# Optimization experiments

Hardware: AMD Instinct MI355X
Metric: run time of the kernel (lower is better)

The kernel has to match this reference:

```python
import jax, jax.numpy as jnp
import numpy as np

ALPHA = 0.01  # 1 / tau, tau=100, dt=None

def setup_inputs() -> dict:
    key = jax.random.key(0)
    ks = jax.random.split(key, 3)
    T, B, I, H = 256, 64, 512, 2048
    x = jax.random.normal(ks[0], (T, B, I), dtype=jnp.float32)
    # PyTorch Linear init scale ~ 1/sqrt(fan_in)
    W_ih = jax.random.normal(ks[1], (H, I), dtype=jnp.float32) / np.sqrt(I)
    b_ih = jnp.zeros((H,), dtype=jnp.float32)
    W_hh = jax.random.normal(ks[2], (H, H), dtype=jnp.float32) / np.sqrt(H)
    b_hh = jnp.zeros((H,), dtype=jnp.float32)
    return {"x": x, "W_ih": W_ih, "b_ih": b_ih, "W_hh": W_hh, "b_hh": b_hh}

def reference(x, W_ih, b_ih, W_hh, b_hh):
    # x: [T, B, I]; leaky CTRNN recurrence, time-major scan.
    T, B, I = x.shape
    H = W_hh.shape[0]
    # Precompute input projection for all timesteps in one GEMM: [T, B, H]
    xin = jnp.einsum('tbi,hi->tbh', x, W_ih) + b_ih
    h0 = jnp.zeros((B, H), dtype=x.dtype)

    def step(h, xt):
        h_new = jax.nn.relu(xt + h @ W_hh.T + b_hh)
        h = (1.0 - ALPHA) * h + ALPHA * h_new
        return h, h

    h_last, out = jax.lax.scan(step, h0, xin)
    return out, h_last
```

## Files before the change

kernel.cpp:

```cpp
#include <hip/hip_runtime.h>

#define T_DIM 256
#define B_DIM 64
#define I_DIM 512
#define H_DIM 2048
#define BH (B_DIM * H_DIM)
#define NBLK 256
#define PUB_U64 32768

typedef __attribute__((ext_vector_type(8))) short bf16x8;
typedef __attribute__((ext_vector_type(4))) float f32x4;

__device__ __forceinline__ unsigned aloadU32(const unsigned* p) {
  return __hip_atomic_load(p, __ATOMIC_RELAXED, __HIP_MEMORY_SCOPE_AGENT);
}
__device__ __forceinline__ unsigned long long aload64(
    const unsigned long long* p) {
  return __hip_atomic_load(p, __ATOMIC_RELAXED, __HIP_MEMORY_SCOPE_AGENT);
}
__device__ __forceinline__ void astore4(float* p, float a) {
  union { unsigned u; float f; } c; c.f = a;
  __hip_atomic_store((unsigned*)p, c.u, __ATOMIC_RELAXED,
                     __HIP_MEMORY_SCOPE_AGENT);
}
__device__ __forceinline__ void astoreU(unsigned long long* p,
                                        unsigned long long v) {
  __hip_atomic_store(p, v, __ATOMIC_RELAXED, __HIP_MEMORY_SCOPE_AGENT);
}

__device__ __forceinline__ unsigned bf16_rne(float x) {
  union { float f; unsigned u; } c; c.f = x;
  return (c.u + 0x7FFFu + ((c.u >> 16) & 1u)) >> 16;
}
__device__ __forceinline__ float bf16_to_f(unsigned b) {
  union { float f; unsigned u; } c; c.u = b << 16; return c.f;
}
__device__ __forceinline__ void cvt_pair(float x0, float x1,
                                         unsigned& hi, unsigned& lo) {
  unsigned h0 = bf16_rne(x0), h1 = bf16_rne(x1);
  float r0 = x0 - bf16_to_f(h0), r1 = x1 - bf16_to_f(h1);
  unsigned l0 = bf16_rne(r0), l1 = bf16_rne(r1);
  hi = h0 | (h1 << 16);
  lo = l0 | (l1 << 16);
}
__device__ __forceinline__ void cvt8(const float* s, uint4& hi, uint4& lo) {
  float4 a = *(const float4*)s;
  float4 b = *(const float4*)(s + 4);
  cvt_pair(a.x, a.y, hi.x, lo.x);
  cvt_pair(a.z, a.w, hi.y, lo.y);
  cvt_pair(b.x, b.y, hi.z, lo.z);
  cvt_pair(b.z, b.w, hi.w, lo.w);
}

__global__ __launch_bounds__(256) void xin_gemm(
    const float* __restrict__ x, const float* __restrict__ Wih,
    const float* __restrict__ bih, const float* __restrict__ bhh,
    float* __restrict__ out)
{
  __shared__ __align__(16) float As[16][132];
  __shared__ __align__(16) float Bs[16][132];
  const int tid = threadIdx.x;
  const int nb = blockIdx.x & 15, mb = blockIdx.x >> 4;
  const int m0 = mb * 128, n0 = nb * 128;
  const int tx = tid & 15, ty = tid >> 4;

  float acc[8][8];
  #pragma unroll
  for (int i = 0; i < 8; ++i)
    #pragma unroll
    for (int j = 0; j < 8; ++j) acc[i][j] = 0.f;

  for (int k0 = 0; k0 < I_DIM; k0 += 16) {
    __syncthreads();
    {
      const int r = tid >> 1;
      #pragma unroll
      for (int c = 0; c < 2; ++c) {
        const int kq = (tid & 1) * 4 + c * 8;
        float4 va = *(const float4*)&x[(size_t)(m0 + r) * I_DIM + k0 + kq];
        As[kq + 0][r] = va.x; As[kq + 1][r] = va.y;
        As[kq + 2][r] = va.z; As[kq + 3][r] = va.w;
        float4 vb = *(const float4*)&Wih[(size_t)(n0 + r) * I_DIM + k0 + kq];
        Bs[kq + 0][r] = vb.x; Bs[kq + 1][r] = vb.y;
        Bs[kq + 2][r] = vb.z; Bs[kq + 3][r] = vb.w;
      }
    }
    __syncthreads();
    #pragma unroll 4
    for (int k = 0; k < 16; ++k) {
      float a[8], b[8];
      *(float4*)&a[0] = *(const float4*)&As[k][ty * 8];
      *(float4*)&a[4] = *(const float4*)&As[k][ty * 8 + 4];
      *(float4*)&b[0] = *(const float4*)&Bs[k][tx * 4];
      *(float4*)&b[4] = *(const float4*)&Bs[k][64 + tx * 4];
      #pragma unroll
      for (int i = 0; i < 8; ++i)
        #pragma unroll
        for (int j = 0; j < 8; ++j) acc[i][j] += a[i] * b[j];
    }
  }

  float bb[8];
  #pragma unroll
  for (int j = 0; j < 4; ++j) {
    bb[j]     = bih[n0 + tx * 4 + j]      + bhh[n0 + tx * 4 + j];
    bb[4 + j] = bih[n0 + 64 + tx * 4 + j] + bhh[n0 + 64 + tx * 4 + j];
  }
  #pragma unroll
  for (int i = 0; i < 8; ++i) {
    const int m = m0 + ty * 8 + i;
    float v[8];
    #pragma unroll
    for (int j = 0; j < 8; ++j) v[j] = acc[i][j] + bb[j];
    if (m < B_DIM) {
      #pragma unroll
      for (int j = 0; j < 8; ++j) v[j] = 0.01f * fmaxf(v[j], 0.f);
    }
    *(float4*)&out[(size_t)m * H_DIM + n0 + tx * 4] =
        make_float4(v[0], v[1], v[2], v[3]);
    *(float4*)&out[(size_t)m * H_DIM + n0 + 64 + tx * 4] =
        make_float4(v[4], v[5], v[6], v[7]);
  }
}

__global__ __launch_bounds__(256) void ctrnn_scan(
    const float* __restrict__ Whh, float* out,
    unsigned long long* __restrict__ pub, unsigned* slots)
{
  __shared__ __align__(16) uint4 Whi[4096];
  __shared__ __align__(16) uint4 Wlo[4096];
  __shared__ __align__(16) f32x4 Red[512];
  __shared__ unsigned short Hs[32][16];

  const int tid = threadIdx.x, bid = blockIdx.x;
  const int nb = bid & 127, bh = bid >> 7;
  const int n0 = nb * 16, b0 = bh * 32;

  const int lane = tid & 63, wid = tid >> 6;
  const int fq = lane >> 4, fr = lane & 15;

  for (int s = tid; s < 4096; s += 256) {
    const int kcg = s >> 6, l = s & 63;
    const int n = n0 + (l & 15), k = kcg * 32 + (l >> 4) * 8;
    uint4 hi, lo;
    cvt8(&Whh[(size_t)n * H_DIM + k], hi, lo);
    Whi[s] = hi; Wlo[s] = lo;
  }

  const int bt = tid >> 7, jh = (tid >> 6) & 1, ln = tid & 63;
  const int rfr = ln & 15, rfq = ln >> 4;
  const int bl0 = bt * 16 + rfq * 4 + jh * 2;
  const size_t oa0 = (size_t)(b0 + bl0) * H_DIM + n0 + rfr;
  const size_t oa1 = oa0 + H_DIM;

  float h0 = out[oa0];
  float h1 = out[oa1];

  Hs[bl0][rfr]     = (unsigned short)bf16_rne(h0);
  Hs[bl0 + 1][rfr] = (unsigned short)bf16_rne(h1);
  __syncthreads();
  if (tid < 64) {
    const int b_l = tid & 31, h8 = tid >> 5;
    const uint4 frag = *(const uint4*)&Hs[b_l][h8 * 8];
    const size_t slot = (size_t)(nb * 2 + h8) * 64 + b0 + b_l;
    astoreU(&pub[slot * 2 + 0], ((const unsigned long long*)&frag)[0]);
    astoreU(&pub[slot * 2 + 1], ((const unsigned long long*)&frag)[1]);
  }
  asm volatile("s_waitcnt vmcnt(0)" ::: "memory");
  if (tid == 0)
    __hip_atomic_store(slots + (size_t)bid * 16, 1u, __ATOMIC_RELAXED,
                       __HIP_MEMORY_SCOPE_AGENT);

  const unsigned* myflag =
      slots + (size_t)(bh * 128 + wid * 32 + (lane & 31)) * 16;

  const int baseA64 = (wid * 4096 + fq * 64 + b0 + fr) * 2;
  const int baseB = wid * 1024;

  for (int t = 1; t < T_DIM; ++t) {
    const float xin0 = out[(size_t)t * BH + oa0];
    const float xin1 = out[(size_t)t * BH + oa1];
    asm volatile("" :: "v"(xin0), "v"(xin1));

    for (int it = 0; it < (1 << 17); ++it) {
      if (__all(aloadU32(myflag) >= (unsigned)t)) break;
      __builtin_amdgcn_s_sleep(1);
    }

    const unsigned long long* pr = pub + (size_t)((t - 1) & 1) * PUB_U64;

    f32x4 acc0 = {0.f, 0.f, 0.f, 0.f}, acc1 = {0.f, 0.f, 0.f, 0.f};
    #pragma unroll
    for (int kc = 0; kc < 16; ++kc) {
      union { unsigned long long u[2]; bf16x8 v; } a0c, a1c;
      a0c.u[0] = aload64(pr + baseA64 + kc * 512 + 0);
      a0c.u[1] = aload64(pr + baseA64 + kc * 512 + 1);
      a1c.u[0] = aload64(pr + baseA64 + kc * 512 + 32);
      a1c.u[1] = aload64(pr + baseA64 + kc * 512 + 33);
      const uint4 bh4 = Whi[baseB + kc * 64 + lane];
      const uint4 bl4 = Wlo[baseB + kc * 64 + lane];
      acc0 = __builtin_amdgcn_mfma_f32_16x16x32_bf16(
          a0c.v, *(const bf16x8*)&bh4, acc0, 0, 0, 0);
      acc0 = __builtin_amdgcn_mfma_f32_16x16x32_bf16(
          a0c.v, *(const bf16x8*)&bl4, acc0, 0, 0, 0);
      acc1 = __builtin_amdgcn_mfma_f32_16x16x32_bf16(
          a1c.v, *(const bf16x8*)&bh4, acc1, 0, 0, 0);
      acc1 = __builtin_amdgcn_mfma_f32_16x16x32_bf16(
          a1c.v, *(const bf16x8*)&bl4, acc1, 0, 0, 0);
    }

    Red[(wid * 2 + 0) * 64 + lane] = acc0;
    Red[(wid * 2 + 1) * 64 + lane] = acc1;
    __syncthreads();

    float s0 = 0.f, s1 = 0.f;
    #pragma unroll
    for (int w = 0; w < 4; ++w) {
      const float2 p = *(const float2*)(
          (const char*)&Red[(w * 2 + bt) * 64 + ln] + jh * 8);
      s0 += p.x; s1 += p.y;
    }

    h0 = 0.99f * h0 + 0.01f * fmaxf(xin0 + s0, 0.f);
    h1 = 0.99f * h1 + 0.01f * fmaxf(xin1 + s1, 0.f);

    astore4(&out[(size_t)t * BH + oa0], h0);
    astore4(&out[(size_t)t * BH + oa1], h1);
    if (t == T_DIM - 1) {
      astore4(&out[(size_t)T_DIM * BH + oa0], h0);
      astore4(&out[(size_t)T_DIM * BH + oa1], h1);
    }

    if (t < T_DIM - 1) {
      __syncthreads();
      Hs[bl0][rfr]     = (unsigned short)bf16_rne(h0);
      Hs[bl0 + 1][rfr] = (unsigned short)bf16_rne(h1);
      __syncthreads();
      if (tid < 64) {
        const int b_l = tid & 31, h8 = tid >> 5;
        const uint4 frag = *(const uint4*)&Hs[b_l][h8 * 8];
        const size_t slot = (size_t)(nb * 2 + h8) * 64 + b0 + b_l;
        unsigned long long* pw =
            pub + (size_t)(t & 1) * PUB_U64 + slot * 2;
        astoreU(pw + 0, ((const unsigned long long*)&frag)[0]);
        astoreU(pw + 1, ((const unsigned long long*)&frag)[1]);
      }
      asm volatile("s_waitcnt vmcnt(0)" ::: "memory");
      if (tid == 0)
        __hip_atomic_store(slots + (size_t)bid * 16, (unsigned)(t + 1),
                           __ATOMIC_RELAXED, __HIP_MEMORY_SCOPE_AGENT);
    }
  }
}

extern "C" void kernel_launch(void* const* d_in, const int* in_sizes, int n_in,
                              void* d_out, int out_size, void* d_ws, size_t ws_size,
                              hipStream_t stream) {
  const float* x    = (const float*)d_in[0];
  const float* Wih  = (const float*)d_in[1];
  const float* bih  = (const float*)d_in[2];
  const float* Whh  = (const float*)d_in[3];
  const float* bhh  = (const float*)d_in[4];
  float* out = (float*)d_out;

  unsigned* slots = (unsigned*)d_ws;
  unsigned long long* pub =
      (unsigned long long*)((char*)d_ws + 32768);

  hipMemsetAsync(d_ws, 0, 32768, stream);

  xin_gemm<<<dim3(2048), dim3(256), 0, stream>>>(x, Wih, bih, bhh, out);
  ctrnn_scan<<<dim3(NBLK), dim3(256), 0, stream>>>(Whh, out, pub, slots);
}
```

Measured before the change: 1.635 ms.

## Read previous hidden state directly from fp32 output instead of bf16 publish buffer

Drops the separate bf16 publish buffer and its shared-memory staging. Each block now reads the previous timestep's fp32 hidden state straight from the output tensor and packs it to bf16 in registers with v_cvt_pk_bf16_f32. This removes two barriers, an LDS round trip and extra global stores per step, but doubles the bytes read per step. The plain (non-atomic) loads of data written by other blocks may also be served stale from non-coherent caches.

```diff
diff --git a/kernel.cpp b/kernel.cpp
--- a/kernel.cpp
+++ b/kernel.cpp
@@ -6,7 +6,6 @@
 #define H_DIM 2048
 #define BH (B_DIM * H_DIM)
 #define NBLK 256
-#define PUB_U64 32768
 
 typedef __attribute__((ext_vector_type(8))) short bf16x8;
 typedef __attribute__((ext_vector_type(4))) float f32x4;
@@ -14,18 +13,22 @@
 __device__ __forceinline__ unsigned aloadU32(const unsigned* p) {
   return __hip_atomic_load(p, __ATOMIC_RELAXED, __HIP_MEMORY_SCOPE_AGENT);
 }
-__device__ __forceinline__ unsigned long long aload64(
-    const unsigned long long* p) {
-  return __hip_atomic_load(p, __ATOMIC_RELAXED, __HIP_MEMORY_SCOPE_AGENT);
+__device__ __forceinline__ float aloadF(const float* p) {
+  union { unsigned u; float f; } c;
+  c.u = __hip_atomic_load((const unsigned*)p, __ATOMIC_RELAXED,
+                          __HIP_MEMORY_SCOPE_AGENT);
+  return c.f;
 }
 __device__ __forceinline__ void astore4(float* p, float a) {
   union { unsigned u; float f; } c; c.f = a;
   __hip_atomic_store((unsigned*)p, c.u, __ATOMIC_RELAXED,
                      __HIP_MEMORY_SCOPE_AGENT);
 }
-__device__ __forceinline__ void astoreU(unsigned long long* p,
-                                        unsigned long long v) {
-  __hip_atomic_store(p, v, __ATOMIC_RELAXED, __HIP_MEMORY_SCOPE_AGENT);
+
+__device__ __forceinline__ unsigned cvtpk(float lo, float hi) {
+  unsigned r;
+  asm("v_cvt_pk_bf16_f32 %0, %1, %2" : "=v"(r) : "v"(lo), "v"(hi));
+  return r;
 }
 
 __device__ __forceinline__ unsigned bf16_rne(float x) {
@@ -124,13 +127,11 @@
 }
 
 __global__ __launch_bounds__(256) void ctrnn_scan(
-    const float* __restrict__ Whh, float* out,
-    unsigned long long* __restrict__ pub, unsigned* slots)
+    const float* __restrict__ Whh, float* out, unsigned* slots)
 {
   __shared__ __align__(16) uint4 Whi[4096];
   __shared__ __align__(16) uint4 Wlo[4096];
   __shared__ __align__(16) f32x4 Red[512];
-  __shared__ unsigned short Hs[32][16];
 
   const int tid = threadIdx.x, bid = blockIdx.x;
   const int nb = bid & 127, bh = bid >> 7;
@@ -153,20 +154,10 @@
   const size_t oa0 = (size_t)(b0 + bl0) * H_DIM + n0 + rfr;
   const size_t oa1 = oa0 + H_DIM;
 
-  float h0 = out[oa0];
-  float h1 = out[oa1];
-
-  Hs[bl0][rfr]     = (unsigned short)bf16_rne(h0);
-  Hs[bl0 + 1][rfr] = (unsigned short)bf16_rne(h1);
+  float h0 = aloadF(&out[oa0]);
+  float h1 = aloadF(&out[oa1]);
+
   __syncthreads();
-  if (tid < 64) {
-    const int b_l = tid & 31, h8 = tid >> 5;
-    const uint4 frag = *(const uint4*)&Hs[b_l][h8 * 8];
-    const size_t slot = (size_t)(nb * 2 + h8) * 64 + b0 + b_l;
-    astoreU(&pub[slot * 2 + 0], ((const unsigned long long*)&frag)[0]);
-    astoreU(&pub[slot * 2 + 1], ((const unsigned long long*)&frag)[1]);
-  }
-  asm volatile("s_waitcnt vmcnt(0)" ::: "memory");
   if (tid == 0)
     __hip_atomic_store(slots + (size_t)bid * 16, 1u, __ATOMIC_RELAXED,
                        __HIP_MEMORY_SCOPE_AGENT);
@@ -174,12 +165,11 @@
   const unsigned* myflag =
       slots + (size_t)(bh * 128 + wid * 32 + (lane & 31)) * 16;
 
-  const int baseA64 = (wid * 4096 + fq * 64 + b0 + fr) * 2;
   const int baseB = wid * 1024;
 
   for (int t = 1; t < T_DIM; ++t) {
-    const float xin0 = out[(size_t)t * BH + oa0];
-    const float xin1 = out[(size_t)t * BH + oa1];
+    const float xin0 = aloadF(&out[(size_t)t * BH + oa0]);
+    const float xin1 = aloadF(&out[(size_t)t * BH + oa1]);
     asm volatile("" :: "v"(xin0), "v"(xin1));
 
     for (int it = 0; it < (1 << 17); ++it) {
@@ -187,26 +177,32 @@
       __builtin_amdgcn_s_sleep(1);
     }
 
-    const unsigned long long* pr = pub + (size_t)((t - 1) & 1) * PUB_U64;
+    const float* hb = out + (size_t)(t - 1) * BH + wid * 512 + fq * 8;
+    const float* hrow0 = hb + (size_t)(b0 + fr) * H_DIM;
+    const float* hrow1 = hb + (size_t)(b0 + 16 + fr) * H_DIM;
 
     f32x4 acc0 = {0.f, 0.f, 0.f, 0.f}, acc1 = {0.f, 0.f, 0.f, 0.f};
     #pragma unroll
     for (int kc = 0; kc < 16; ++kc) {
-      union { unsigned long long u[2]; bf16x8 v; } a0c, a1c;
-      a0c.u[0] = aload64(pr + baseA64 + kc * 512 + 0);
-      a0c.u[1] = aload64(pr + baseA64 + kc * 512 + 1);
-      a1c.u[0] = aload64(pr + baseA64 + kc * 512 + 32);
-      a1c.u[1] = aload64(pr + baseA64 + kc * 512 + 33);
+      const float4 x0 = *(const float4*)(hrow0 + kc * 32);
+      const float4 x1 = *(const float4*)(hrow0 + kc * 32 + 4);
+      const float4 y0 = *(const float4*)(hrow1 + kc * 32);
+      const float4 y1 = *(const float4*)(hrow1 + kc * 32 + 4);
+      union { unsigned w[4]; bf16x8 v; } a0, a1;
+      a0.w[0] = cvtpk(x0.x, x0.y); a0.w[1] = cvtpk(x0.z, x0.w);
+      a0.w[2] = cvtpk(x1.x, x1.y); a0.w[3] = cvtpk(x1.z, x1.w);
+      a1.w[0] = cvtpk(y0.x, y0.y); a1.w[1] = cvtpk(y0.z, y0.w);
+      a1.w[2] = cvtpk(y1.x, y1.y); a1.w[3] = cvtpk(y1.z, y1.w);
       const uint4 bh4 = Whi[baseB + kc * 64 + lane];
       const uint4 bl4 = Wlo[baseB + kc * 64 + lane];
       acc0 = __builtin_amdgcn_mfma_f32_16x16x32_bf16(
-          a0c.v, *(const bf16x8*)&bh4, acc0, 0, 0, 0);
+          a0.v, *(const bf16x8*)&bh4, acc0, 0, 0, 0);
       acc0 = __builtin_amdgcn_mfma_f32_16x16x32_bf16(
-          a0c.v, *(const bf16x8*)&bl4, acc0, 0, 0, 0);
+          a0.v, *(const bf16x8*)&bl4, acc0, 0, 0, 0);
       acc1 = __builtin_amdgcn_mfma_f32_16x16x32_bf16(
-          a1c.v, *(const bf16x8*)&bh4, acc1, 0, 0, 0);
+          a1.v, *(const bf16x8*)&bh4, acc1, 0, 0, 0);
       acc1 = __builtin_amdgcn_mfma_f32_16x16x32_bf16(
-          a1c.v, *(const bf16x8*)&bl4, acc1, 0, 0, 0);
+          a1.v, *(const bf16x8*)&bl4, acc1, 0, 0, 0);
     }
 
     Red[(wid * 2 + 0) * 64 + lane] = acc0;
@@ -229,23 +225,9 @@
     if (t == T_DIM - 1) {
       astore4(&out[(size_t)T_DIM * BH + oa0], h0);
       astore4(&out[(size_t)T_DIM * BH + oa1], h1);
-    }
-
-    if (t < T_DIM - 1) {
+    } else {
+      asm volatile("s_waitcnt vmcnt(0)" ::: "memory");
       __syncthreads();
-      Hs[bl0][rfr]     = (unsigned short)bf16_rne(h0);
-      Hs[bl0 + 1][rfr] = (unsigned short)bf16_rne(h1);
-      __syncthreads();
-      if (tid < 64) {
-        const int b_l = tid & 31, h8 = tid >> 5;
-        const uint4 frag = *(const uint4*)&Hs[b_l][h8 * 8];
-        const size_t slot = (size_t)(nb * 2 + h8) * 64 + b0 + b_l;
-        unsigned long long* pw =
-            pub + (size_t)(t & 1) * PUB_U64 + slot * 2;
-        astoreU(pw + 0, ((const unsigned long long*)&frag)[0]);
-        astoreU(pw + 1, ((const unsigned long long*)&frag)[1]);
-      }
-      asm volatile("s_waitcnt vmcnt(0)" ::: "memory");
       if (tid == 0)
         __hip_atomic_store(slots + (size_t)bid * 16, (unsigned)(t + 1),
                            __ATOMIC_RELAXED, __HIP_MEMORY_SCOPE_AGENT);
@@ -264,11 +246,9 @@
   float* out = (float*)d_out;
 
   unsigned* slots = (unsigned*)d_ws;
-  unsigned long long* pub =
-      (unsigned long long*)((char*)d_ws + 32768);
 
   hipMemsetAsync(d_ws, 0, 32768, stream);
 
   xin_gemm<<<dim3(2048), dim3(256), 0, stream>>>(x, Wih, bih, bhh, out);
-  ctrnn_scan<<<dim3(NBLK), dim3(256), 0, stream>>>(Whh, out, pub, slots);
-}
+  ctrnn_scan<<<dim3(NBLK), dim3(256), 0, stream>>>(Whh, out, slots);
+}
```

Result: slower. 2.840 ms (+73.7%).

## Use split-bf16 MFMA for the input projection GEMM

Applied to the files above, without the earlier changes.

Replaces the FP32 SIMT register-tiled input-projection GEMM with an MFMA bf16 kernel. Each fp32 operand is split into hi/lo bf16 parts, and three MFMAs per tile pair (hi*hi, hi*lo, lo*hi) approximate fp32 accuracy. The goal is to cut the cost of the large T*B x H x I projection, which runs before the sequential scan. In exchange it adds conversion work during shared-memory staging, and the output stores become scalar and strided rather than float4.

```diff
diff --git a/kernel.cpp b/kernel.cpp
--- a/kernel.cpp
+++ b/kernel.cpp
@@ -57,70 +57,82 @@
     const float* __restrict__ bih, const float* __restrict__ bhh,
     float* __restrict__ out)
 {
-  __shared__ __align__(16) float As[16][132];
-  __shared__ __align__(16) float Bs[16][132];
+  __shared__ __align__(16) uint4 Xhi[512], Xlo[512];
+  __shared__ __align__(16) uint4 Ghi[512], Glo[512];
+
   const int tid = threadIdx.x;
   const int nb = blockIdx.x & 15, mb = blockIdx.x >> 4;
   const int m0 = mb * 128, n0 = nb * 128;
-  const int tx = tid & 15, ty = tid >> 4;
-
-  float acc[8][8];
+  const int lane = tid & 63, wid = tid >> 6;
+  const int wm = wid & 1, wn = wid >> 1;
+  const int fq = lane >> 4, fr = lane & 15;
+
+  f32x4 acc[4][4];
   #pragma unroll
-  for (int i = 0; i < 8; ++i)
-    #pragma unroll
-    for (int j = 0; j < 8; ++j) acc[i][j] = 0.f;
-
-  for (int k0 = 0; k0 < I_DIM; k0 += 16) {
+  for (int i = 0; i < 4; ++i)
+    #pragma unroll
+    for (int j = 0; j < 4; ++j) acc[i][j] = (f32x4){0.f, 0.f, 0.f, 0.f};
+
+  for (int k0 = 0; k0 < I_DIM; k0 += 32) {
     __syncthreads();
-    {
-      const int r = tid >> 1;
+    #pragma unroll
+    for (int h = 0; h < 2; ++h) {
+      const int f = tid + h * 256;
+      const int r = f >> 2, o = f & 3;
+      const int s = (r >> 4) * 64 + o * 16 + (r & 15);
+      uint4 hi, lo;
+      cvt8(&x[(size_t)(m0 + r) * I_DIM + k0 + o * 8], hi, lo);
+      Xhi[s] = hi; Xlo[s] = lo;
+      cvt8(&Wih[(size_t)(n0 + r) * I_DIM + k0 + o * 8], hi, lo);
+      Ghi[s] = hi; Glo[s] = lo;
+    }
+    __syncthreads();
+
+    uint4 ahi[4], alo[4];
+    #pragma unroll
+    for (int mt = 0; mt < 4; ++mt) {
+      ahi[mt] = Xhi[(wm * 4 + mt) * 64 + lane];
+      alo[mt] = Xlo[(wm * 4 + mt) * 64 + lane];
+    }
+    #pragma unroll
+    for (int nt = 0; nt < 4; ++nt) {
+      const uint4 bhv = Ghi[(wn * 4 + nt) * 64 + lane];
+      const uint4 blv = Glo[(wn * 4 + nt) * 64 + lane];
       #pragma unroll
-      for (int c = 0; c < 2; ++c) {
-        const int kq = (tid & 1) * 4 + c * 8;
-        float4 va = *(const float4*)&x[(size_t)(m0 + r) * I_DIM + k0 + kq];
-        As[kq + 0][r] = va.x; As[kq + 1][r] = va.y;
-        As[kq + 2][r] = va.z; As[kq + 3][r] = va.w;
-        float4 vb = *(const float4*)&Wih[(size_t)(n0 + r) * I_DIM + k0 + kq];
-        Bs[kq + 0][r] = vb.x; Bs[kq + 1][r] = vb.y;
-        Bs[kq + 2][r] = vb.z; Bs[kq + 3][r] = vb.w;
+      for (int mt = 0; mt < 4; ++mt) {
+        acc[mt][nt] = __builtin_amdgcn_mfma_f32_16x16x32_bf16(
+            *(const bf16x8*)&ahi[mt], *(const bf16x8*)&bhv, acc[mt][nt],
+            0, 0, 0);
+        acc[mt][nt] = __builtin_amdgcn_mfma_f32_16x16x32_bf16(
+            *(const bf16x8*)&ahi[mt], *(const bf16x8*)&blv, acc[mt][nt],
+            0, 0, 0);
+        acc[mt][nt] = __builtin_amdgcn_mfma_f32_16x16x32_bf16(
+            *(const bf16x8*)&alo[mt], *(const bf16x8*)&bhv, acc[mt][nt],
+            0, 0, 0);
       }
     }
-    __syncthreads();
-    #pragma unroll 4
-    for (int k = 0; k < 16; ++k) {
-      float a[8], b[8];
-      *(float4*)&a[0] = *(const float4*)&As[k][ty * 8];
-      *(float4*)&a[4] = *(const float4*)&As[k][ty * 8 + 4];
-      *(float4*)&b[0] = *(const float4*)&Bs[k][tx * 4];
-      *(float4*)&b[4] = *(const float4*)&Bs[k][64 + tx * 4];
+  }
+
+  float bb[4];
+  #pragma unroll
+  for (int nt = 0; nt < 4; ++nt) {
+    const int n = n0 + wn * 64 + nt * 16 + fr;
+    bb[nt] = bih[n] + bhh[n];
+  }
+  #pragma unroll
+  for (int mt = 0; mt < 4; ++mt)
+    #pragma unroll
+    for (int j = 0; j < 4; ++j) {
+      const int m = m0 + wm * 64 + mt * 16 + fq * 4 + j;
+      const bool fold = (m < B_DIM);
       #pragma unroll
-      for (int i = 0; i < 8; ++i)
-        #pragma unroll
-        for (int j = 0; j < 8; ++j) acc[i][j] += a[i] * b[j];
-    }
-  }
-
-  float bb[8];
-  #pragma unroll
-  for (int j = 0; j < 4; ++j) {
-    bb[j]     = bih[n0 + tx * 4 + j]      + bhh[n0 + tx * 4 + j];
-    bb[4 + j] = bih[n0 + 64 + tx * 4 + j] + bhh[n0 + 64 + tx * 4 + j];
-  }
-  #pragma unroll
-  for (int i = 0; i < 8; ++i) {
-    const int m = m0 + ty * 8 + i;
-    float v[8];
-    #pragma unroll
-    for (int j = 0; j < 8; ++j) v[j] = acc[i][j] + bb[j];
-    if (m < B_DIM) {
-      #pragma unroll
-      for (int j = 0; j < 8; ++j) v[j] = 0.01f * fmaxf(v[j], 0.f);
-    }
-    *(float4*)&out[(size_t)m * H_DIM + n0 + tx * 4] =
-        make_float4(v[0], v[1], v[2], v[3]);
-    *(float4*)&out[(size_t)m * H_DIM + n0 + 64 + tx * 4] =
-        make_float4(v[4], v[5], v[6], v[7]);
-  }
+      for (int nt = 0; nt < 4; ++nt) {
+        const int n = n0 + wn * 64 + nt * 16 + fr;
+        float v = acc[mt][nt][j] + bb[nt];
+        if (fold) v = 0.01f * fmaxf(v, 0.f);
+        out[(size_t)m * H_DIM + n] = v;
+      }
+    }
 }
 
 __global__ __launch_bounds__(256) void ctrnn_scan(
```

After: 1.396 ms (median of 2 runs). -14.7%, faster.
